# Performance work log

Hardware: AMD Instinct MI355X
Metric: run time of the kernel (lower is better)

Reference implementation:

```python
import jax, jax.numpy as jnp
import numpy as np

B, L, N, H, D, TOPK = 32, 720, 512, 16, 64, 8
TEMP = 1.0


def setup_inputs() -> dict:
    key = jax.random.key(0)
    ks = jax.random.split(key, 18)
    s = lambda k, shp, fan: jax.random.normal(k, shp, jnp.float32) / np.sqrt(fan)
    return {
        'x': jax.random.normal(ks[0], (B, L, N), jnp.float32),
        'var_embed': s(ks[1], (N, H), H),
        'Wq': s(ks[2], (H, H), H), 'bq': jnp.zeros((H,), jnp.float32),
        'Wk': s(ks[3], (H, H), H), 'bk': jnp.zeros((H,), jnp.float32),
        'Wscore': s(ks[4], (N, 1), N), 'bscore': jnp.zeros((1,), jnp.float32),
        'Wc1': s(ks[5], (N, D), N), 'bc1': jnp.zeros((D,), jnp.float32),
        'Wc2': s(ks[6], (D, D), D), 'bc2': jnp.zeros((D,), jnp.float32),
        'Wcn': s(ks[7], (D, N), D), 'bcn': jnp.zeros((N,), jnp.float32),
        'Wg': s(ks[8], (2 * N, N), 2 * N), 'bg': jnp.zeros((N,), jnp.float32),
        'Wf': s(ks[9], (N, N), N), 'bf': jnp.zeros((N,), jnp.float32),
        'gamma': jnp.ones((N,), jnp.float32), 'beta': jnp.zeros((N,), jnp.float32),
    }


def _forward(x, var_embed, Wq, bq, Wk, bk, Wscore, bscore, Wc1, bc1, Wc2, bc2,
             Wcn, bcn, Wg, bg, Wf, bf, gamma, beta):
    # --- SparseVariableRouter (eval mode: no gumbel noise) ---
    Q = var_embed @ Wq + bq          # [N,H]
    K = var_embed @ Wk + bk          # [N,H]
    sim = Q @ K.T                    # [N,N] (identical across batch in torch)
    eye = jnp.eye(N, dtype=bool)
    sim = jnp.where(eye, -1e9, sim)
    topk_vals, topk_idx = jax.lax.top_k(sim, TOPK)      # [N,k]
    w = jax.nn.softmax(topk_vals / TEMP, axis=-1)        # [N,k]
    x_perm = jnp.transpose(x, (0, 2, 1))                 # [B,N,L]
    neighbors = x_perm[:, topk_idx, :]                   # [B,N,k,L] gather
    ring_out = jnp.einsum('bnkl,nk->bln', neighbors, w)  # [B,L,N]
    # --- center path ---
    attn = jax.nn.softmax(x @ Wscore + bscore, axis=1)   # [B,L,1] softmax over L
    center_raw = jnp.sum(x * attn, axis=1)               # [B,N]
    c = jax.nn.gelu(center_raw @ Wc1 + bc1, approximate=False)
    c = jax.nn.gelu(c @ Wc2 + bc2, approximate=False)
    center = c @ Wcn + bcn                               # [B,N]
    center_b = jnp.broadcast_to(center[:, None, :], (x.shape[0], x.shape[1], N))
    # --- gated fusion + residual LN ---
    gate = jax.nn.sigmoid(jnp.concatenate([ring_out, center_b], axis=-1) @ Wg + bg)
    fused = gate * ring_out + (1.0 - gate) * center_b
    fused = fused @ Wf + bf
    h = fused + x
    mu = jnp.mean(h, axis=-1, keepdims=True)
    var = jnp.var(h, axis=-1, keepdims=True)
    return (h - mu) * jax.lax.rsqrt(var + 1e-5) * gamma + beta


def reference(x, var_embed, Wq, bq, Wk, bk, Wscore, bscore, Wc1, bc1, Wc2, bc2,
              Wcn, bcn, Wg, bg, Wf, bf, gamma, beta):
    return _forward(x, var_embed, Wq, bq, Wk, bk, Wscore, bscore, Wc1, bc1,
                    Wc2, bc2, Wcn, bcn, Wg, bg, Wf, bf, gamma, beta)
```

## Files before the change

### kernel.cpp

```cpp
#include <hip/hip_runtime.h>
#include <hip/hip_bf16.h>
#include <math.h>

#define B_ 32
#define L_ 720
#define N_ 512
#define H_ 16
#define D_ 64
#define TOPK_ 8
#define M_ (B_ * L_)
#define RPB 8
#define CRCH 16
#define CRL (L_ / CRCH)

typedef __bf16 bf16x8 __attribute__((ext_vector_type(8)));
typedef float f32x16 __attribute__((ext_vector_type(16)));

__device__ __forceinline__ void async_cp16(const __hip_bfloat16* g, __hip_bfloat16* l) {
    __builtin_amdgcn_global_load_lds(
        (const __attribute__((address_space(1))) void*)g,
        (__attribute__((address_space(3))) void*)l, 16, 0, 0);
}

__device__ __forceinline__ bf16x8 frag_ld(const __hip_bfloat16* base, int row, int j0) {
    return *(const bf16x8*)(base + row * 64 + (((j0) ^ (row & 7)) << 3));
}

__global__ __launch_bounds__(512) void qk_kernel(
    const float* __restrict__ ve,
    const float* __restrict__ Wq, const float* __restrict__ bq,
    const float* __restrict__ Wk, const float* __restrict__ bk,
    float* __restrict__ Qm, float* __restrict__ Km)
{
    const int g = blockIdx.x * 512 + threadIdx.x;
    const int j = g >> 4, h = g & 15;
    const float* vr = ve + j * H_;
    float q = bq[h], k = bk[h];
    #pragma unroll
    for (int m = 0; m < H_; ++m) {
        const float v = vr[m];
        q += v * Wq[m * H_ + h];
        k += v * Wk[m * H_ + h];
    }
    Qm[g] = q;
    Km[g] = k;
}

__global__ __launch_bounds__(64) void topk_kernel(
    const float* __restrict__ Qm, const float* __restrict__ Km,
    float* __restrict__ w_out, int* __restrict__ idx_out)
{
    const int n = blockIdx.x;
    const int lane = threadIdx.x;

    float4 q0, q1, q2, q3;
    {
        const float4* qr = (const float4*)(Qm + n * H_);
        q0 = qr[0]; q1 = qr[1]; q2 = qr[2]; q3 = qr[3];
    }

    float sv[8]; int si[8];
    #pragma unroll
    for (int c = 0; c < 8; ++c) {
        const int j = c * 64 + lane;
        const float4* kr = (const float4*)(Km + j * H_);
        float4 k0 = kr[0], k1 = kr[1], k2 = kr[2], k3 = kr[3];
        float s = q0.x * k0.x + q0.y * k0.y + q0.z * k0.z + q0.w * k0.w
                + q1.x * k1.x + q1.y * k1.y + q1.z * k1.z + q1.w * k1.w
                + q2.x * k2.x + q2.y * k2.y + q2.z * k2.z + q2.w * k2.w
                + q3.x * k3.x + q3.y * k3.y + q3.z * k3.z + q3.w * k3.w;
        sv[c] = (j == n) ? -1e9f : s;
        si[c] = j;
    }

    float keepv[TOPK_]; int keepi[TOPK_];
    #pragma unroll
    for (int k = 0; k < TOPK_; ++k) {
        float bv = sv[0]; int bi = si[0]; int bslot = 0;
        #pragma unroll
        for (int c = 1; c < 8; ++c)
            if (sv[c] > bv || (sv[c] == bv && si[c] < bi)) { bv = sv[c]; bi = si[c]; bslot = c; }
        float v = bv; int i = bi;
        #pragma unroll
        for (int off = 32; off > 0; off >>= 1) {
            float v2 = __shfl_xor(v, off);
            int   i2 = __shfl_xor(i, off);
            if (v2 > v || (v2 == v && i2 < i)) { v = v2; i = i2; }
        }
        keepv[k] = v; keepi[k] = i;
        if (i == bi) sv[bslot] = -INFINITY;
    }

    if (lane == 0) {
        float vmax = keepv[0];
        float ev[TOPK_], esum = 0.f;
        #pragma unroll
        for (int k = 0; k < TOPK_; k++) { ev[k] = expf(keepv[k] - vmax); esum += ev[k]; }
        float inv = 1.f / esum;
        #pragma unroll
        for (int k = 0; k < TOPK_; k++) {
            w_out[n * TOPK_ + k] = ev[k] * inv;
            idx_out[n * TOPK_ + k] = keepi[k];
        }
    }
}

__global__ __launch_bounds__(512) void ring_kernel(
    const float* __restrict__ x, const float* __restrict__ w,
    const int* __restrict__ idx,
    const float* __restrict__ Wscore, const float* __restrict__ bscore,
    __hip_bfloat16* __restrict__ ring, float* __restrict__ s)
{
    __shared__ float xs[RPB][N_];
    __shared__ float wsh[N_ * TOPK_];
    __shared__ int   ish[N_ * TOPK_];
    const int t = threadIdx.x;
    const int row0 = blockIdx.x * RPB;

    for (int i = t; i < N_ * TOPK_; i += 512) { wsh[i] = w[i]; ish[i] = idx[i]; }
    {
        const float4* xg = (const float4*)(x + (size_t)row0 * N_);
        float4* xsf = (float4*)&xs[0][0];
        xsf[t] = xg[t];
        xsf[t + 512] = xg[t + 512];
    }
    __syncthreads();

    {
        const int wv = t >> 6, lane = t & 63;
        float sa = 0.f;
        #pragma unroll
        for (int i = 0; i < 8; ++i) sa += xs[wv][lane + i * 64] * Wscore[lane + i * 64];
        for (int off = 32; off > 0; off >>= 1) sa += __shfl_down(sa, off);
        if (lane == 0) s[row0 + wv] = sa + bscore[0];
    }

    float wr[TOPK_]; int ir[TOPK_];
    #pragma unroll
    for (int k = 0; k < TOPK_; ++k) { wr[k] = wsh[t * TOPK_ + k]; ir[k] = ish[t * TOPK_ + k]; }
    #pragma unroll
    for (int r = 0; r < RPB; ++r) {
        float acc = 0.f;
        #pragma unroll
        for (int k = 0; k < TOPK_; ++k) acc += wr[k] * xs[r][ir[k]];
        ring[(size_t)(row0 + r) * N_ + t] = __float2bfloat16(acc);
    }
}

__global__ __launch_bounds__(256) void attn_softmax_kernel(float* __restrict__ s)
{
    const int b = blockIdx.x;
    const int t = threadIdx.x;
    float* row = s + (size_t)b * L_;

    __shared__ float sm[4];
    __shared__ float sm2[4];

    float lmax = -1e30f;
    for (int l = t; l < L_; l += 256) lmax = fmaxf(lmax, row[l]);
    for (int off = 32; off > 0; off >>= 1) lmax = fmaxf(lmax, __shfl_down(lmax, off));
    if ((t & 63) == 0) sm[t >> 6] = lmax;
    __syncthreads();
    float gmax = fmaxf(fmaxf(sm[0], sm[1]), fmaxf(sm[2], sm[3]));

    float lsum = 0.f;
    for (int l = t; l < L_; l += 256) {
        float e = expf(row[l] - gmax);
        row[l] = e;
        lsum += e;
    }
    for (int off = 32; off > 0; off >>= 1) lsum += __shfl_down(lsum, off);
    if ((t & 63) == 0) sm2[t >> 6] = lsum;
    __syncthreads();
    float inv = 1.f / (sm2[0] + sm2[1] + sm2[2] + sm2[3]);
    for (int l = t; l < L_; l += 256) row[l] *= inv;
}

__global__ __launch_bounds__(512) void center_raw_kernel(
    const float* __restrict__ x, const float* __restrict__ attn,
    float* __restrict__ craw_p)
{
    const int b = blockIdx.x >> 4;
    const int c = blockIdx.x & 15;
    const int n = threadIdx.x;
    __shared__ float ash[CRL];
    const int l0 = c * CRL;
    if (n < CRL) ash[n] = attn[b * L_ + l0 + n];
    __syncthreads();
    const float* xb = x + ((size_t)b * L_ + l0) * N_;
    float acc = 0.f;
    #pragma unroll 3
    for (int l = 0; l < CRL; l++) acc += ash[l] * xb[(size_t)l * N_ + n];
    craw_p[(size_t)(b * CRCH + c) * N_ + n] = acc;
}

__device__ __forceinline__ float gelu_exact(float v) {
    return 0.5f * v * (1.0f + erff(v * 0.70710678118654752440f));
}

__global__ __launch_bounds__(512) void center_mlp_kernel(
    const float* __restrict__ craw_p,
    const float* __restrict__ Wc1, const float* __restrict__ bc1,
    const float* __restrict__ Wc2, const float* __restrict__ bc2,
    const float* __restrict__ Wcn, const float* __restrict__ bcn,
    float* __restrict__ center)
{
    const int b = blockIdx.x;
    const int t = threadIdx.x;
    const int col = t & 63;
    const int seg = t >> 6;
    __shared__ float cr[N_];
    __shared__ float psum[8][D_];
    __shared__ float h1[D_];
    __shared__ float h2[D_];

    {
        float acc = 0.f;
        #pragma unroll
        for (int c = 0; c < CRCH; ++c) acc += craw_p[(size_t)(b * CRCH + c) * N_ + t];
        cr[t] = acc;
    }
    __syncthreads();
    {
        float p = 0.f;
        #pragma unroll 8
        for (int m = seg * 64; m < seg * 64 + 64; ++m) p += cr[m] * Wc1[m * D_ + col];
        psum[seg][col] = p;
    }
    __syncthreads();
    if (t < D_) {
        float acc = bc1[t];
        #pragma unroll
        for (int s2 = 0; s2 < 8; ++s2) acc += psum[s2][t];
        h1[t] = gelu_exact(acc);
    }
    __syncthreads();
    if (t < D_) {
        float acc = bc2[t];
        #pragma unroll 8
        for (int j = 0; j < D_; j++) acc += h1[j] * Wc2[j * D_ + t];
        h2[t] = gelu_exact(acc);
    }
    __syncthreads();
    {
        float acc = bcn[t];
        #pragma unroll 8
        for (int j = 0; j < D_; j++) acc += h2[j] * Wcn[j * N_ + t];
        center[b * N_ + t] = acc;
    }
}

__global__ __launch_bounds__(512) void cg_kernel(
    const float* __restrict__ center, const float* __restrict__ Wg,
    const float* __restrict__ bg, float* __restrict__ cg)
{
    const int nc = blockIdx.x;
    const int b  = blockIdx.y;
    const int t  = threadIdx.x;
    const int col = nc * 64 + (t & 63);
    const int seg = t >> 6;
    __shared__ float cs[N_];
    __shared__ float psum[8][64];

    cs[t] = center[b * N_ + t];
    __syncthreads();
    {
        float p = 0.f;
        const float* wp = Wg + (size_t)(N_ + seg * 64) * N_ + col;
        #pragma unroll 8
        for (int m = 0; m < 64; ++m) { p += cs[seg * 64 + m] * wp[0]; wp += N_; }
        psum[seg][t & 63] = p;
    }
    __syncthreads();
    if (t < 64) {
        float acc = bg[nc * 64 + t];
        #pragma unroll
        for (int s2 = 0; s2 < 8; ++s2) acc += psum[s2][t];
        cg[b * N_ + nc * 64 + t] = acc;
    }
}

__global__ __launch_bounds__(256) void convert_kernel(
    const float* __restrict__ Wg, const float* __restrict__ Wf,
    __hip_bfloat16* __restrict__ WgT, __hip_bfloat16* __restrict__ WfT)
{
    const int n = blockIdx.x & 511;
    const bool isf = blockIdx.x >= 512;
    const float* src = isf ? Wf : Wg;
    __hip_bfloat16* dst = isf ? WfT : WgT;
    for (int k = threadIdx.x; k < N_; k += 256)
        dst[n * N_ + k] = __float2bfloat16(src[(size_t)k * N_ + n]);
}

#define GEMM_BODY(EPILOGUE)                                                    \
    __shared__ __hip_bfloat16 Ash[64 * 64];                                    \
    __shared__ __hip_bfloat16 Bsh[64 * 64];                                    \
    const int tid  = threadIdx.x;                                              \
    const int lane = tid & 63;                                                 \
    const int wv   = tid >> 6;                                                 \
    const int m32  = lane & 31;                                                \
    const int half = lane >> 5;                                                \
    const int wr   = wv >> 1;                                                  \
    const int wc   = wv & 1;                                                   \
    const int row0 = blockIdx.x * 64;                                          \
    const int n0   = blockIdx.y * 64;                                          \
    const int swz  = (lane & 7) ^ (lane >> 3);                                 \
    const int rln  = lane >> 3;                                                \
    f32x16 acc;                                                                \
    _Pragma("unroll") for (int e = 0; e < 16; e++) acc[e] = 0.f;               \
    for (int step = 0; step < 8; ++step) {                                     \
        const int k0 = step * 64;                                              \
        const __hip_bfloat16* Ab = A  + (size_t)row0 * N_ + k0 + swz * 8;      \
        const __hip_bfloat16* Bb = BT + (size_t)n0   * N_ + k0 + swz * 8;      \
        __syncthreads();                                                       \
        _Pragma("unroll") for (int j = 0; j < 2; ++j) {                        \
            const int r = j * 32 + wv * 8 + rln;                               \
            const int lb = (j * 256 + wv * 64) * 8;                            \
            async_cp16(Ab + (size_t)r * N_, Ash + lb);                         \
            async_cp16(Bb + (size_t)r * N_, Bsh + lb);                         \
        }                                                                      \
        __syncthreads();                                                       \
        _Pragma("unroll") for (int ks = 0; ks < 4; ++ks) {                     \
            const int j0 = ks * 2 + half;                                      \
            bf16x8 a0 = frag_ld(Ash, wr * 32 + m32, j0);                       \
            bf16x8 b0 = frag_ld(Bsh, wc * 32 + m32, j0);                       \
            acc = __builtin_amdgcn_mfma_f32_32x32x16_bf16(a0, b0, acc, 0, 0, 0); \
        }                                                                      \
    }                                                                          \
    _Pragma("unroll") for (int reg = 0; reg < 16; ++reg) {                     \
        const int rg  = row0 + wr * 32 +                                       \
                        (reg & 3) + 8 * (reg >> 2) + 4 * half;                 \
        const int col = n0 + wc * 32 + m32;                                    \
        const float aval = acc[reg];                                           \
        EPILOGUE                                                               \
    }

__global__ __launch_bounds__(256) void gemm_gate_kernel(
    const __hip_bfloat16* __restrict__ A,
    const __hip_bfloat16* __restrict__ BT,
    const float* __restrict__ cg,
    const float* __restrict__ center,
    __hip_bfloat16* __restrict__ fused)
{
    GEMM_BODY({
        const int b = rg / L_;
        const float logit = aval + cg[b * N_ + col];
        const float g = 1.f / (1.f + expf(-logit));
        const float rv = __bfloat162float(A[(size_t)rg * N_ + col]);
        const float f = g * rv + (1.f - g) * center[b * N_ + col];
        fused[(size_t)rg * N_ + col] = __float2bfloat16(f);
    })
}

__global__ __launch_bounds__(256) void gemm_out_kernel(
    const __hip_bfloat16* __restrict__ A,
    const __hip_bfloat16* __restrict__ BT,
    const float* __restrict__ x,
    const float* __restrict__ bfv,
    float* __restrict__ out)
{
    GEMM_BODY({
        out[(size_t)rg * N_ + col] = aval + bfv[col] + x[(size_t)rg * N_ + col];
    })
}

__global__ __launch_bounds__(512) void ln_kernel(
    float* __restrict__ out,
    const float* __restrict__ gamma, const float* __restrict__ beta)
{
    const int tid = threadIdx.x;
    const int r = tid >> 7;
    const int c = tid & 127;
    const int row = blockIdx.x * 4 + r;
    const int wid = tid >> 6;
    __shared__ float ls[8], lq[8];

    float4 v = ((const float4*)(out + (size_t)row * N_))[c];
    float sum = v.x + v.y + v.z + v.w;
    float sq  = v.x * v.x + v.y * v.y + v.z * v.z + v.w * v.w;
    for (int off = 32; off > 0; off >>= 1) {
        sum += __shfl_down(sum, off);
        sq  += __shfl_down(sq,  off);
    }
    if ((tid & 63) == 0) { ls[wid] = sum; lq[wid] = sq; }
    __syncthreads();
    const float S  = ls[2 * r] + ls[2 * r + 1];
    const float Q2 = lq[2 * r] + lq[2 * r + 1];
    const float mu  = S * (1.0f / N_);
    const float var = Q2 * (1.0f / N_) - mu * mu;
    const float inv = 1.0f / sqrtf(var + 1e-5f);
    const float4 g4 = ((const float4*)gamma)[c];
    const float4 b4 = ((const float4*)beta)[c];
    float4 o;
    o.x = (v.x - mu) * inv * g4.x + b4.x;
    o.y = (v.y - mu) * inv * g4.y + b4.y;
    o.z = (v.z - mu) * inv * g4.z + b4.z;
    o.w = (v.w - mu) * inv * g4.w + b4.w;
    ((float4*)(out + (size_t)row * N_))[c] = o;
}

extern "C" void kernel_launch(void* const* d_in, const int* in_sizes, int n_in,
                              void* d_out, int out_size, void* d_ws, size_t ws_size,
                              hipStream_t stream) {
    const float* x       = (const float*)d_in[0];
    const float* ve      = (const float*)d_in[1];
    const float* Wq      = (const float*)d_in[2];
    const float* bq      = (const float*)d_in[3];
    const float* Wk      = (const float*)d_in[4];
    const float* bk      = (const float*)d_in[5];
    const float* Wscore  = (const float*)d_in[6];
    const float* bscore  = (const float*)d_in[7];
    const float* Wc1     = (const float*)d_in[8];
    const float* bc1     = (const float*)d_in[9];
    const float* Wc2     = (const float*)d_in[10];
    const float* bc2     = (const float*)d_in[11];
    const float* Wcn     = (const float*)d_in[12];
    const float* bcn     = (const float*)d_in[13];
    const float* Wg      = (const float*)d_in[14];
    const float* bg      = (const float*)d_in[15];
    const float* Wf      = (const float*)d_in[16];
    const float* bf      = (const float*)d_in[17];
    const float* gamma   = (const float*)d_in[18];
    const float* beta    = (const float*)d_in[19];
    float* out = (float*)d_out;

    char* p = (char*)d_ws;
    float* ws_w    = (float*)p; p += N_ * TOPK_ * sizeof(float);
    int*   ws_idx  = (int*)p;   p += N_ * TOPK_ * sizeof(int);
    float* ws_s    = (float*)p; p += B_ * L_ * sizeof(float);
    float* ws_crp  = (float*)p; p += B_ * CRCH * N_ * sizeof(float);
    float* ws_cent = (float*)p; p += B_ * N_ * sizeof(float);
    float* ws_cg   = (float*)p; p += B_ * N_ * sizeof(float);
    float* ws_Q    = (float*)p; p += N_ * H_ * sizeof(float);
    float* ws_K    = (float*)p; p += N_ * H_ * sizeof(float);
    __hip_bfloat16* ws_ring  = (__hip_bfloat16*)p; p += (size_t)M_ * N_ * sizeof(__hip_bfloat16);
    __hip_bfloat16* ws_fused = (__hip_bfloat16*)p; p += (size_t)M_ * N_ * sizeof(__hip_bfloat16);
    __hip_bfloat16* ws_WgT   = (__hip_bfloat16*)p; p += (size_t)N_ * N_ * sizeof(__hip_bfloat16);
    __hip_bfloat16* ws_WfT   = (__hip_bfloat16*)p; p += (size_t)N_ * N_ * sizeof(__hip_bfloat16);

    convert_kernel<<<1024, 256, 0, stream>>>(Wg, Wf, ws_WgT, ws_WfT);
    qk_kernel<<<16, 512, 0, stream>>>(ve, Wq, bq, Wk, bk, ws_Q, ws_K);
    topk_kernel<<<N_, 64, 0, stream>>>(ws_Q, ws_K, ws_w, ws_idx);
    ring_kernel<<<M_ / RPB, 512, 0, stream>>>(x, ws_w, ws_idx, Wscore, bscore,
                                              ws_ring, ws_s);
    attn_softmax_kernel<<<B_, 256, 0, stream>>>(ws_s);
    center_raw_kernel<<<B_ * CRCH, 512, 0, stream>>>(x, ws_s, ws_crp);
    center_mlp_kernel<<<B_, 512, 0, stream>>>(ws_crp, Wc1, bc1, Wc2, bc2,
                                              Wcn, bcn, ws_cent);
    cg_kernel<<<dim3(8, B_), 512, 0, stream>>>(ws_cent, Wg, bg, ws_cg);
    dim3 ggrid(M_ / 64, N_ / 64);
    gemm_gate_kernel<<<ggrid, 256, 0, stream>>>(ws_ring, ws_WgT, ws_cg,
                                                ws_cent, ws_fused);
    gemm_out_kernel<<<ggrid, 256, 0, stream>>>(ws_fused, ws_WfT, x, bf, out);
    ln_kernel<<<M_ / 4, 512, 0, stream>>>(out, gamma, beta);
}
```

Baseline: 273.2 us.

## Fuse gate GEMM, output GEMM and LayerNorm into one row-block kernel

```diff
diff --git a/kernel.cpp b/kernel.cpp
--- a/kernel.cpp
+++ b/kernel.cpp
@@ -12,19 +12,19 @@
 #define RPB 8
 #define CRCH 16
 #define CRL (L_ / CRCH)
+#define PROWS 32
 
 typedef __bf16 bf16x8 __attribute__((ext_vector_type(8)));
 typedef float f32x16 __attribute__((ext_vector_type(16)));
 
-__device__ __forceinline__ void async_cp16(const __hip_bfloat16* g, __hip_bfloat16* l) {
-    __builtin_amdgcn_global_load_lds(
-        (const __attribute__((address_space(1))) void*)g,
-        (__attribute__((address_space(3))) void*)l, 16, 0, 0);
-}
-
-__device__ __forceinline__ bf16x8 frag_ld(const __hip_bfloat16* base, int row, int j0) {
-    return *(const bf16x8*)(base + row * 64 + (((j0) ^ (row & 7)) << 3));
-}
+__device__ __forceinline__ f32x16 fzero16() {
+    f32x16 z;
+    #pragma unroll
+    for (int e = 0; e < 16; ++e) z[e] = 0.f;
+    return z;
+}
+
+__device__ __forceinline__ float sigm(float v) { return 1.f / (1.f + expf(-v)); }
 
 __global__ __launch_bounds__(512) void qk_kernel(
     const float* __restrict__ ve,
@@ -292,111 +292,162 @@
         dst[n * N_ + k] = __float2bfloat16(src[(size_t)k * N_ + n]);
 }
 
-#define GEMM_BODY(EPILOGUE)                                                    \
-    __shared__ __hip_bfloat16 Ash[64 * 64];                                    \
-    __shared__ __hip_bfloat16 Bsh[64 * 64];                                    \
-    const int tid  = threadIdx.x;                                              \
-    const int lane = tid & 63;                                                 \
-    const int wv   = tid >> 6;                                                 \
-    const int m32  = lane & 31;                                                \
-    const int half = lane >> 5;                                                \
-    const int wr   = wv >> 1;                                                  \
-    const int wc   = wv & 1;                                                   \
-    const int row0 = blockIdx.x * 64;                                          \
-    const int n0   = blockIdx.y * 64;                                          \
-    const int swz  = (lane & 7) ^ (lane >> 3);                                 \
-    const int rln  = lane >> 3;                                                \
-    f32x16 acc;                                                                \
-    _Pragma("unroll") for (int e = 0; e < 16; e++) acc[e] = 0.f;               \
-    for (int step = 0; step < 8; ++step) {                                     \
-        const int k0 = step * 64;                                              \
-        const __hip_bfloat16* Ab = A  + (size_t)row0 * N_ + k0 + swz * 8;      \
-        const __hip_bfloat16* Bb = BT + (size_t)n0   * N_ + k0 + swz * 8;      \
-        __syncthreads();                                                       \
-        _Pragma("unroll") for (int j = 0; j < 2; ++j) {                        \
-            const int r = j * 32 + wv * 8 + rln;                               \
-            const int lb = (j * 256 + wv * 64) * 8;                            \
-            async_cp16(Ab + (size_t)r * N_, Ash + lb);                         \
-            async_cp16(Bb + (size_t)r * N_, Bsh + lb);                         \
-        }                                                                      \
-        __syncthreads();                                                       \
-        _Pragma("unroll") for (int ks = 0; ks < 4; ++ks) {                     \
-            const int j0 = ks * 2 + half;                                      \
-            bf16x8 a0 = frag_ld(Ash, wr * 32 + m32, j0);                       \
-            bf16x8 b0 = frag_ld(Bsh, wc * 32 + m32, j0);                       \
-            acc = __builtin_amdgcn_mfma_f32_32x32x16_bf16(a0, b0, acc, 0, 0, 0); \
-        }                                                                      \
-    }                                                                          \
-    _Pragma("unroll") for (int reg = 0; reg < 16; ++reg) {                     \
-        const int rg  = row0 + wr * 32 +                                       \
-                        (reg & 3) + 8 * (reg >> 2) + 4 * half;                 \
-        const int col = n0 + wc * 32 + m32;                                    \
-        const float aval = acc[reg];                                           \
-        EPILOGUE                                                               \
-    }
-
-__global__ __launch_bounds__(256) void gemm_gate_kernel(
-    const __hip_bfloat16* __restrict__ A,
-    const __hip_bfloat16* __restrict__ BT,
+__global__ __launch_bounds__(256) void fused_tail_kernel(
+    const __hip_bfloat16* __restrict__ ring,
+    const __hip_bfloat16* __restrict__ WgT,
+    const __hip_bfloat16* __restrict__ WfT,
     const float* __restrict__ cg,
     const float* __restrict__ center,
-    __hip_bfloat16* __restrict__ fused)
-{
-    GEMM_BODY({
-        const int b = rg / L_;
-        const float logit = aval + cg[b * N_ + col];
-        const float g = 1.f / (1.f + expf(-logit));
-        const float rv = __bfloat162float(A[(size_t)rg * N_ + col]);
-        const float f = g * rv + (1.f - g) * center[b * N_ + col];
-        fused[(size_t)rg * N_ + col] = __float2bfloat16(f);
-    })
-}
-
-__global__ __launch_bounds__(256) void gemm_out_kernel(
-    const __hip_bfloat16* __restrict__ A,
-    const __hip_bfloat16* __restrict__ BT,
     const float* __restrict__ x,
     const float* __restrict__ bfv,
+    const float* __restrict__ gamma,
+    const float* __restrict__ beta,
     float* __restrict__ out)
 {
-    GEMM_BODY({
-        out[(size_t)rg * N_ + col] = aval + bfv[col] + x[(size_t)rg * N_ + col];
-    })
-}
-
-__global__ __launch_bounds__(512) void ln_kernel(
-    float* __restrict__ out,
-    const float* __restrict__ gamma, const float* __restrict__ beta)
-{
-    const int tid = threadIdx.x;
-    const int r = tid >> 7;
-    const int c = tid & 127;
-    const int row = blockIdx.x * 4 + r;
-    const int wid = tid >> 6;
-    __shared__ float ls[8], lq[8];
-
-    float4 v = ((const float4*)(out + (size_t)row * N_))[c];
-    float sum = v.x + v.y + v.z + v.w;
-    float sq  = v.x * v.x + v.y * v.y + v.z * v.z + v.w * v.w;
-    for (int off = 32; off > 0; off >>= 1) {
-        sum += __shfl_down(sum, off);
-        sq  += __shfl_down(sq,  off);
-    }
-    if ((tid & 63) == 0) { ls[wid] = sum; lq[wid] = sq; }
-    __syncthreads();
-    const float S  = ls[2 * r] + ls[2 * r + 1];
-    const float Q2 = lq[2 * r] + lq[2 * r + 1];
+    __shared__ __attribute__((aligned(16))) __hip_bfloat16 fsh[PROWS * N_];
+    __shared__ __attribute__((aligned(16))) float cgs[2][N_];
+    __shared__ __attribute__((aligned(16))) float cents[2][N_];
+    __shared__ __attribute__((aligned(16))) float bfs[N_];
+    __shared__ __attribute__((aligned(16))) float gms[N_];
+    __shared__ __attribute__((aligned(16))) float bts[N_];
+    __shared__ float ps[4][PROWS];
+    __shared__ float pq[4][PROWS];
+
+    const int tid  = threadIdx.x;
+    const int wv   = tid >> 6;
+    const int lane = tid & 63;
+    const int m    = lane & 31;
+    const int half = lane >> 5;
+    const int row0 = blockIdx.x * PROWS;
+    const int b0   = row0 / L_;
+    const int b1   = (row0 + PROWS - 1) / L_;
+    const int rowg = row0 + m;
+    const int bsel = (rowg / L_ != b0) ? 1 : 0;
+
+    for (int i = tid; i < N_; i += 256) {
+        cgs[0][i]   = cg[b0 * N_ + i];
+        cgs[1][i]   = cg[b1 * N_ + i];
+        cents[0][i] = center[b0 * N_ + i];
+        cents[1][i] = center[b1 * N_ + i];
+        bfs[i] = bfv[i];
+        gms[i] = gamma[i];
+        bts[i] = beta[i];
+    }
+
+    f32x16 ac0 = fzero16(), ac1 = fzero16(), ac2 = fzero16(), ac3 = fzero16();
+    {
+        const __hip_bfloat16* rb = ring + (size_t)rowg * N_ + half * 8;
+        const __hip_bfloat16* w0 = WgT + (size_t)(( 0 + wv) * 32 + m) * N_ + half * 8;
+        const __hip_bfloat16* w1 = WgT + (size_t)(( 4 + wv) * 32 + m) * N_ + half * 8;
+        const __hip_bfloat16* w2 = WgT + (size_t)(( 8 + wv) * 32 + m) * N_ + half * 8;
+        const __hip_bfloat16* w3 = WgT + (size_t)((12 + wv) * 32 + m) * N_ + half * 8;
+        #pragma unroll 4
+        for (int kc = 0; kc < 32; ++kc) {
+            const int off = kc * 16;
+            const bf16x8 b = *(const bf16x8*)(rb + off);
+            ac0 = __builtin_amdgcn_mfma_f32_32x32x16_bf16(*(const bf16x8*)(w0 + off), b, ac0, 0, 0, 0);
+            ac1 = __builtin_amdgcn_mfma_f32_32x32x16_bf16(*(const bf16x8*)(w1 + off), b, ac1, 0, 0, 0);
+            ac2 = __builtin_amdgcn_mfma_f32_32x32x16_bf16(*(const bf16x8*)(w2 + off), b, ac2, 0, 0, 0);
+            ac3 = __builtin_amdgcn_mfma_f32_32x32x16_bf16(*(const bf16x8*)(w3 + off), b, ac3, 0, 0, 0);
+        }
+    }
+    __syncthreads();
+
+#define GEPI(AC, G)                                                            \
+    {                                                                          \
+        const int ntb = ((G) * 4 + wv) * 32;                                   \
+        _Pragma("unroll") for (int q = 0; q < 4; ++q) {                        \
+            const int nb = ntb + 8 * q + 4 * half;                             \
+            const float4 cgq = *(const float4*)&cgs[bsel][nb];                 \
+            const float4 ctq = *(const float4*)&cents[bsel][nb];               \
+            const uint2 rvp = *(const uint2*)(ring + (size_t)rowg * N_ + nb);  \
+            const float rv0 = __uint_as_float((rvp.x & 0xffffu) << 16);        \
+            const float rv1 = __uint_as_float((rvp.x >> 16) << 16);            \
+            const float rv2 = __uint_as_float((rvp.y & 0xffffu) << 16);        \
+            const float rv3 = __uint_as_float((rvp.y >> 16) << 16);            \
+            const float g0 = sigm(AC[4 * q + 0] + cgq.x);                      \
+            const float g1 = sigm(AC[4 * q + 1] + cgq.y);                      \
+            const float g2 = sigm(AC[4 * q + 2] + cgq.z);                      \
+            const float g3 = sigm(AC[4 * q + 3] + cgq.w);                      \
+            const float f0 = g0 * rv0 + (1.f - g0) * ctq.x;                    \
+            const float f1 = g1 * rv1 + (1.f - g1) * ctq.y;                    \
+            const float f2 = g2 * rv2 + (1.f - g2) * ctq.z;                    \
+            const float f3 = g3 * rv3 + (1.f - g3) * ctq.w;                    \
+            uint2 wpk;                                                         \
+            wpk.x = (unsigned)__builtin_bit_cast(unsigned short, __float2bfloat16(f0)) |        \
+                    ((unsigned)__builtin_bit_cast(unsigned short, __float2bfloat16(f1)) << 16); \
+            wpk.y = (unsigned)__builtin_bit_cast(unsigned short, __float2bfloat16(f2)) |        \
+                    ((unsigned)__builtin_bit_cast(unsigned short, __float2bfloat16(f3)) << 16); \
+            *(uint2*)((char*)fsh + m * 1024 + (((nb >> 3) ^ (m & 7)) << 4) + ((nb & 7) << 1)) = wpk; \
+        }                                                                      \
+    }
+    GEPI(ac0, 0) GEPI(ac1, 1) GEPI(ac2, 2) GEPI(ac3, 3)
+    __syncthreads();
+
+    f32x16 oc0 = fzero16(), oc1 = fzero16(), oc2 = fzero16(), oc3 = fzero16();
+    {
+        const char* fb = (const char*)fsh + m * 1024;
+        const __hip_bfloat16* v0 = WfT + (size_t)(( 0 + wv) * 32 + m) * N_ + half * 8;
+        const __hip_bfloat16* v1 = WfT + (size_t)(( 4 + wv) * 32 + m) * N_ + half * 8;
+        const __hip_bfloat16* v2 = WfT + (size_t)(( 8 + wv) * 32 + m) * N_ + half * 8;
+        const __hip_bfloat16* v3 = WfT + (size_t)((12 + wv) * 32 + m) * N_ + half * 8;
+        #pragma unroll 4
+        for (int kc = 0; kc < 32; ++kc) {
+            const int c8 = kc * 2 + half;
+            const bf16x8 b = *(const bf16x8*)(fb + ((c8 ^ (m & 7)) << 4));
+            const int off = kc * 16;
+            oc0 = __builtin_amdgcn_mfma_f32_32x32x16_bf16(*(const bf16x8*)(v0 + off), b, oc0, 0, 0, 0);
+            oc1 = __builtin_amdgcn_mfma_f32_32x32x16_bf16(*(const bf16x8*)(v1 + off), b, oc1, 0, 0, 0);
+            oc2 = __builtin_amdgcn_mfma_f32_32x32x16_bf16(*(const bf16x8*)(v2 + off), b, oc2, 0, 0, 0);
+            oc3 = __builtin_amdgcn_mfma_f32_32x32x16_bf16(*(const bf16x8*)(v3 + off), b, oc3, 0, 0, 0);
+        }
+    }
+
+    float lsum = 0.f, lsq = 0.f;
+#define OEPI(AC, G)                                                            \
+    {                                                                          \
+        const int ntb = ((G) * 4 + wv) * 32;                                   \
+        _Pragma("unroll") for (int q = 0; q < 4; ++q) {                        \
+            const int nb = ntb + 8 * q + 4 * half;                             \
+            const float4 bq = *(const float4*)&bfs[nb];                        \
+            const float4 xq = *(const float4*)(x + (size_t)rowg * N_ + nb);    \
+            AC[4 * q + 0] += bq.x + xq.x;                                      \
+            AC[4 * q + 1] += bq.y + xq.y;                                      \
+            AC[4 * q + 2] += bq.z + xq.z;                                      \
+            AC[4 * q + 3] += bq.w + xq.w;                                      \
+            lsum += AC[4 * q + 0] + AC[4 * q + 1] + AC[4 * q + 2] + AC[4 * q + 3]; \
+            lsq  += AC[4 * q + 0] * AC[4 * q + 0] + AC[4 * q + 1] * AC[4 * q + 1]  \
+                  + AC[4 * q + 2] * AC[4 * q + 2] + AC[4 * q + 3] * AC[4 * q + 3]; \
+        }                                                                      \
+    }
+    OEPI(oc0, 0) OEPI(oc1, 1) OEPI(oc2, 2) OEPI(oc3, 3)
+
+    lsum += __shfl_xor(lsum, 32);
+    lsq  += __shfl_xor(lsq, 32);
+    if (half == 0) { ps[wv][m] = lsum; pq[wv][m] = lsq; }
+    __syncthreads();
+    const float S   = ps[0][m] + ps[1][m] + ps[2][m] + ps[3][m];
+    const float Q2  = pq[0][m] + pq[1][m] + pq[2][m] + pq[3][m];
     const float mu  = S * (1.0f / N_);
     const float var = Q2 * (1.0f / N_) - mu * mu;
-    const float inv = 1.0f / sqrtf(var + 1e-5f);
-    const float4 g4 = ((const float4*)gamma)[c];
-    const float4 b4 = ((const float4*)beta)[c];
-    float4 o;
-    o.x = (v.x - mu) * inv * g4.x + b4.x;
-    o.y = (v.y - mu) * inv * g4.y + b4.y;
-    o.z = (v.z - mu) * inv * g4.z + b4.z;
-    o.w = (v.w - mu) * inv * g4.w + b4.w;
-    ((float4*)(out + (size_t)row * N_))[c] = o;
+    const float inv = rsqrtf(var + 1e-5f);
+
+#define LSTORE(AC, G)                                                          \
+    {                                                                          \
+        const int ntb = ((G) * 4 + wv) * 32;                                   \
+        _Pragma("unroll") for (int q = 0; q < 4; ++q) {                        \
+            const int nb = ntb + 8 * q + 4 * half;                             \
+            const float4 g4 = *(const float4*)&gms[nb];                        \
+            const float4 b4 = *(const float4*)&bts[nb];                        \
+            float4 o;                                                          \
+            o.x = (AC[4 * q + 0] - mu) * inv * g4.x + b4.x;                    \
+            o.y = (AC[4 * q + 1] - mu) * inv * g4.y + b4.y;                    \
+            o.z = (AC[4 * q + 2] - mu) * inv * g4.z + b4.z;                    \
+            o.w = (AC[4 * q + 3] - mu) * inv * g4.w + b4.w;                    \
+            *(float4*)(out + (size_t)rowg * N_ + nb) = o;                      \
+        }                                                                      \
+    }
+    LSTORE(oc0, 0) LSTORE(oc1, 1) LSTORE(oc2, 2) LSTORE(oc3, 3)
 }
 
 extern "C" void kernel_launch(void* const* d_in, const int* in_sizes, int n_in,
@@ -434,7 +485,6 @@
     float* ws_Q    = (float*)p; p += N_ * H_ * sizeof(float);
     float* ws_K    = (float*)p; p += N_ * H_ * sizeof(float);
     __hip_bfloat16* ws_ring  = (__hip_bfloat16*)p; p += (size_t)M_ * N_ * sizeof(__hip_bfloat16);
-    __hip_bfloat16* ws_fused = (__hip_bfloat16*)p; p += (size_t)M_ * N_ * sizeof(__hip_bfloat16);
     __hip_bfloat16* ws_WgT   = (__hip_bfloat16*)p; p += (size_t)N_ * N_ * sizeof(__hip_bfloat16);
     __hip_bfloat16* ws_WfT   = (__hip_bfloat16*)p; p += (size_t)N_ * N_ * sizeof(__hip_bfloat16);
 
@@ -448,9 +498,7 @@
     center_mlp_kernel<<<B_, 512, 0, stream>>>(ws_crp, Wc1, bc1, Wc2, bc2,
                                               Wcn, bcn, ws_cent);
     cg_kernel<<<dim3(8, B_), 512, 0, stream>>>(ws_cent, Wg, bg, ws_cg);
-    dim3 ggrid(M_ / 64, N_ / 64);
-    gemm_gate_kernel<<<ggrid, 256, 0, stream>>>(ws_ring, ws_WgT, ws_cg,
-                                                ws_cent, ws_fused);
-    gemm_out_kernel<<<ggrid, 256, 0, stream>>>(ws_fused, ws_WfT, x, bf, out);
-    ln_kernel<<<M_ / 4, 512, 0, stream>>>(out, gamma, beta);
-}
+    fused_tail_kernel<<<M_ / PROWS, 256, 0, stream>>>(ws_ring, ws_WgT, ws_WfT,
+                                                      ws_cg, ws_cent, x, bf,
+                                                      gamma, beta, out);
+}
```

New measurement: 309.1 us. +13.1%, slower.

## Fuse output GEMM with residual add and LayerNorm over full-row tiles

Applied to the files above, without the earlier changes.

```diff
diff --git a/kernel.cpp b/kernel.cpp
--- a/kernel.cpp
+++ b/kernel.cpp
@@ -12,6 +12,7 @@
 #define RPB 8
 #define CRCH 16
 #define CRL (L_ / CRCH)
+#define OROWS 64
 
 typedef __bf16 bf16x8 __attribute__((ext_vector_type(8)));
 typedef float f32x16 __attribute__((ext_vector_type(16)));
@@ -24,6 +25,13 @@
 
 __device__ __forceinline__ bf16x8 frag_ld(const __hip_bfloat16* base, int row, int j0) {
     return *(const bf16x8*)(base + row * 64 + (((j0) ^ (row & 7)) << 3));
+}
+
+__device__ __forceinline__ f32x16 fzero16() {
+    f32x16 z;
+    #pragma unroll
+    for (int e = 0; e < 16; ++e) z[e] = 0.f;
+    return z;
 }
 
 __global__ __launch_bounds__(512) void qk_kernel(
@@ -352,51 +360,128 @@
     })
 }
 
-__global__ __launch_bounds__(256) void gemm_out_kernel(
+__global__ __launch_bounds__(512) void gemm_out_ln_kernel(
     const __hip_bfloat16* __restrict__ A,
     const __hip_bfloat16* __restrict__ BT,
     const float* __restrict__ x,
     const float* __restrict__ bfv,
+    const float* __restrict__ gamma,
+    const float* __restrict__ beta,
     float* __restrict__ out)
 {
-    GEMM_BODY({
-        out[(size_t)rg * N_ + col] = aval + bfv[col] + x[(size_t)rg * N_ + col];
-    })
-}
-
-__global__ __launch_bounds__(512) void ln_kernel(
-    float* __restrict__ out,
-    const float* __restrict__ gamma, const float* __restrict__ beta)
-{
-    const int tid = threadIdx.x;
-    const int r = tid >> 7;
-    const int c = tid & 127;
-    const int row = blockIdx.x * 4 + r;
-    const int wid = tid >> 6;
-    __shared__ float ls[8], lq[8];
-
-    float4 v = ((const float4*)(out + (size_t)row * N_))[c];
-    float sum = v.x + v.y + v.z + v.w;
-    float sq  = v.x * v.x + v.y * v.y + v.z * v.z + v.w * v.w;
-    for (int off = 32; off > 0; off >>= 1) {
-        sum += __shfl_down(sum, off);
-        sq  += __shfl_down(sq,  off);
-    }
-    if ((tid & 63) == 0) { ls[wid] = sum; lq[wid] = sq; }
-    __syncthreads();
-    const float S  = ls[2 * r] + ls[2 * r + 1];
-    const float Q2 = lq[2 * r] + lq[2 * r + 1];
-    const float mu  = S * (1.0f / N_);
-    const float var = Q2 * (1.0f / N_) - mu * mu;
-    const float inv = 1.0f / sqrtf(var + 1e-5f);
-    const float4 g4 = ((const float4*)gamma)[c];
-    const float4 b4 = ((const float4*)beta)[c];
-    float4 o;
-    o.x = (v.x - mu) * inv * g4.x + b4.x;
-    o.y = (v.y - mu) * inv * g4.y + b4.y;
-    o.z = (v.z - mu) * inv * g4.z + b4.z;
-    o.w = (v.w - mu) * inv * g4.w + b4.w;
-    ((float4*)(out + (size_t)row * N_))[c] = o;
+    __shared__ __hip_bfloat16 Wsh[512 * 64];
+    __shared__ __hip_bfloat16 Dsh[64 * 64];
+    __shared__ float ps[8][2][32];
+    __shared__ float pq[8][2][32];
+
+    const int tid  = threadIdx.x;
+    const int lane = tid & 63;
+    const int wv8  = tid >> 6;
+    const int m32  = lane & 31;
+    const int half = lane >> 5;
+    const int row0 = blockIdx.x * OROWS;
+    const int swz  = (lane & 7) ^ (lane >> 3);
+    const int rln  = lane >> 3;
+
+    f32x16 acc[2][2];
+    #pragma unroll
+    for (int g = 0; g < 2; ++g)
+        #pragma unroll
+        for (int i = 0; i < 2; ++i) acc[g][i] = fzero16();
+
+    for (int step = 0; step < 8; ++step) {
+        const int k0 = step * 64;
+        __syncthreads();
+        #pragma unroll
+        for (int j = 0; j < 8; ++j) {
+            const int r = j * 64 + wv8 * 8 + rln;
+            async_cp16(BT + (size_t)r * N_ + k0 + swz * 8,
+                       Wsh + (j * 512 + wv8 * 64) * 8);
+        }
+        {
+            const int r = wv8 * 8 + rln;
+            async_cp16(A + (size_t)(row0 + r) * N_ + k0 + swz * 8,
+                       Dsh + (wv8 * 64) * 8);
+        }
+        __syncthreads();
+        #pragma unroll
+        for (int ks = 0; ks < 4; ++ks) {
+            const int j0 = ks * 2 + half;
+            bf16x8 d0 = frag_ld(Dsh, m32, j0);
+            bf16x8 d1 = frag_ld(Dsh, 32 + m32, j0);
+            bf16x8 wa = frag_ld(Wsh, (wv8 * 2 + 0) * 32 + m32, j0);
+            bf16x8 wb = frag_ld(Wsh, (wv8 * 2 + 1) * 32 + m32, j0);
+            acc[0][0] = __builtin_amdgcn_mfma_f32_32x32x16_bf16(wa, d0, acc[0][0], 0, 0, 0);
+            acc[0][1] = __builtin_amdgcn_mfma_f32_32x32x16_bf16(wb, d0, acc[0][1], 0, 0, 0);
+            acc[1][0] = __builtin_amdgcn_mfma_f32_32x32x16_bf16(wa, d1, acc[1][0], 0, 0, 0);
+            acc[1][1] = __builtin_amdgcn_mfma_f32_32x32x16_bf16(wb, d1, acc[1][1], 0, 0, 0);
+        }
+    }
+
+    float ls[2] = {0.f, 0.f};
+    float lq[2] = {0.f, 0.f};
+    #pragma unroll
+    for (int g = 0; g < 2; ++g) {
+        const int rowg = row0 + g * 32 + m32;
+        #pragma unroll
+        for (int i = 0; i < 2; ++i) {
+            const int ntb = (wv8 * 2 + i) * 32;
+            #pragma unroll
+            for (int q = 0; q < 4; ++q) {
+                const int nb = ntb + 8 * q + 4 * half;
+                const float4 bq = *(const float4*)(bfv + nb);
+                const float4 xq = *(const float4*)(x + (size_t)rowg * N_ + nb);
+                float v0 = acc[g][i][4 * q + 0] + bq.x + xq.x;
+                float v1 = acc[g][i][4 * q + 1] + bq.y + xq.y;
+                float v2 = acc[g][i][4 * q + 2] + bq.z + xq.z;
+                float v3 = acc[g][i][4 * q + 3] + bq.w + xq.w;
+                acc[g][i][4 * q + 0] = v0;
+                acc[g][i][4 * q + 1] = v1;
+                acc[g][i][4 * q + 2] = v2;
+                acc[g][i][4 * q + 3] = v3;
+                ls[g] += v0 + v1 + v2 + v3;
+                lq[g] += v0 * v0 + v1 * v1 + v2 * v2 + v3 * v3;
+            }
+        }
+    }
+
+    #pragma unroll
+    for (int g = 0; g < 2; ++g) {
+        ls[g] += __shfl_xor(ls[g], 32);
+        lq[g] += __shfl_xor(lq[g], 32);
+    }
+    if (half == 0) {
+        ps[wv8][0][m32] = ls[0]; pq[wv8][0][m32] = lq[0];
+        ps[wv8][1][m32] = ls[1]; pq[wv8][1][m32] = lq[1];
+    }
+    __syncthreads();
+
+    #pragma unroll
+    for (int g = 0; g < 2; ++g) {
+        float S = 0.f, Q2 = 0.f;
+        #pragma unroll
+        for (int w = 0; w < 8; ++w) { S += ps[w][g][m32]; Q2 += pq[w][g][m32]; }
+        const float mu  = S * (1.0f / N_);
+        const float var = Q2 * (1.0f / N_) - mu * mu;
+        const float inv = rsqrtf(var + 1e-5f);
+        const int rowg = row0 + g * 32 + m32;
+        #pragma unroll
+        for (int i = 0; i < 2; ++i) {
+            const int ntb = (wv8 * 2 + i) * 32;
+            #pragma unroll
+            for (int q = 0; q < 4; ++q) {
+                const int nb = ntb + 8 * q + 4 * half;
+                const float4 g4 = *(const float4*)(gamma + nb);
+                const float4 b4 = *(const float4*)(beta + nb);
+                float4 o;
+                o.x = (acc[g][i][4 * q + 0] - mu) * inv * g4.x + b4.x;
+                o.y = (acc[g][i][4 * q + 1] - mu) * inv * g4.y + b4.y;
+                o.z = (acc[g][i][4 * q + 2] - mu) * inv * g4.z + b4.z;
+                o.w = (acc[g][i][4 * q + 3] - mu) * inv * g4.w + b4.w;
+                *(float4*)(out + (size_t)rowg * N_ + nb) = o;
+            }
+        }
+    }
 }
 
 extern "C" void kernel_launch(void* const* d_in, const int* in_sizes, int n_in,
@@ -451,6 +536,6 @@
     dim3 ggrid(M_ / 64, N_ / 64);
     gemm_gate_kernel<<<ggrid, 256, 0, stream>>>(ws_ring, ws_WgT, ws_cg,
                                                 ws_cent, ws_fused);
-    gemm_out_kernel<<<ggrid, 256, 0, stream>>>(ws_fused, ws_WfT, x, bf, out);
-    ln_kernel<<<M_ / 4, 512, 0, stream>>>(out, gamma, beta);
-}
+    gemm_out_ln_kernel<<<M_ / OROWS, 512, 0, stream>>>(ws_fused, ws_WfT, x, bf,
+                                                       gamma, beta, out);
+}
```

After: 267.1 us. 1.02x faster.
